# Optimization experiments

Measured on AMD Instinct MI355X. Metric: run time of the kernel, lower is better.

The kernel has to match this reference:

```python
import jax, jax.numpy as jnp
from jax import lax
import numpy as np

D = 1024   # hidden_size
N = 8      # num_experts
K = 2      # num_chosen_experts
KS = 1     # num_shared_experts
H = 2 * D  # hidden_ratio * D
B, S = 2, 1024


def setup_inputs() -> dict:
    key = jax.random.key(0)
    k1, k2, k3, k4 = jax.random.split(key, 4)
    scale = 1.0 / np.sqrt(D).astype(np.float32)
    x = jax.random.normal(k1, (B, S, D), dtype=jnp.float32)
    Wg = jax.random.normal(k2, (D, N), dtype=jnp.float32) * scale
    Wl1 = jax.random.normal(k3, (N, D, 2 * H), dtype=jnp.float32) * scale
    Wl2 = jax.random.normal(k4, (N, H, D), dtype=jnp.float32) * scale
    return {"x_BSD": x, "Wg_DN": Wg, "Wl1_ND2H": Wl1, "Wl2_NHD": Wl2}


def _moe(x_BSD, Wg_DN, Wl1_ND2H, Wl2_NHD):
    b, s, d = x_BSD.shape
    x_MD = x_BSD.reshape(b * s, d)            # [M, D]
    Nr = N - KS                               # number of routed experts

    # --- gating (softmax path) ---
    s_raw_MN = x_MD @ Wg_DN                   # [M, N]
    routed = jax.nn.softmax(s_raw_MN[:, :Nr].astype(jnp.float32), axis=-1)
    shared = jax.nn.softmax(s_raw_MN[:, Nr:].astype(jnp.float32), axis=-1)

    # biases for routed experts are zero at init -> topk on raw softmax scores
    _, idx_MK = lax.top_k(routed, K - KS)     # [M, K-KS]
    mask = jnp.sum(jax.nn.one_hot(idx_MK, Nr, dtype=jnp.float32), axis=1)  # [M, Nr]
    sel = routed * mask
    routed_n = sel / jnp.sum(sel, axis=-1, keepdims=True)   # renormalize selected gates
    shared_n = shared / jnp.sum(shared, axis=-1, keepdims=True)
    gates_MN = jnp.concatenate([routed_n, shared_n], axis=-1).astype(x_MD.dtype)  # [M, N]

    # --- experts: gather-free dense combine; gates are exactly 0 for unselected experts ---
    def step(y_MD, inp):
        w1_D2H, w2_HD, g_M = inp
        z = x_MD @ w1_D2H                     # [M, 2H]
        a, bgate = jnp.split(z, 2, axis=-1)
        h = jax.nn.silu(bgate) * a            # SwiGLU
        return y_MD + g_M[:, None] * (h @ w2_HD), None

    y0 = jnp.zeros_like(x_MD)
    y_MD, _ = lax.scan(step, y0, (Wl1_ND2H, Wl2_NHD, gates_MN.T))
    return y_MD.reshape(b, s, d)


def reference(x_BSD, Wg_DN, Wl1_ND2H, Wl2_NHD):
    return _moe(x_BSD, Wg_DN, Wl1_ND2H, Wl2_NHD)
```

## Files before the change

kernel.cpp:

```cpp
#include <hip/hip_runtime.h>
#include <stdint.h>


typedef __bf16 bf16x8 __attribute__((ext_vector_type(8)));
typedef float f32x4 __attribute__((ext_vector_type(4)));

typedef __attribute__((address_space(1))) const void gvoid_t;
typedef __attribute__((address_space(3))) void lvoid_t;

__device__ __forceinline__ void gload16(void* lds, const void* g) {
  __builtin_amdgcn_global_load_lds((gvoid_t*)g, (lvoid_t*)lds, 16, 0, 0);
}

__device__ __forceinline__ uint16_t f2bf(float f) {
  union { float f; uint32_t u; } v; v.f = f;
  uint32_t u = v.u + 0x7fffu + ((v.u >> 16) & 1u);
  return (uint16_t)(u >> 16);
}

#define S_VMCNT12() asm volatile("s_waitcnt vmcnt(12)" ::: "memory")
#define S_VMCNT16() asm volatile("s_waitcnt vmcnt(16)" ::: "memory")
#define S_VMCNT0()  asm volatile("s_waitcnt vmcnt(0)" ::: "memory")
#define S_LGKM0()   asm volatile("s_waitcnt lgkmcnt(0)" ::: "memory")
#define S_BAR()     __builtin_amdgcn_s_barrier()

#define CVT_PK(dst, lo, hi) \
  asm("v_cvt_pk_bf16_f32 %0, %1, %2" : "=v"(dst) : "v"(lo), "v"(hi))

__global__ __launch_bounds__(256) void gate_kernel(const float* __restrict__ x,
                                                   const float* __restrict__ Wg,
                                                   uint16_t* __restrict__ xbf,
                                                   int* __restrict__ idx) {
  int wid = threadIdx.x >> 6, lane = threadIdx.x & 63;
  int m = blockIdx.x * 4 + wid;
  const float* xr = x + (size_t)m * 1024;
  uint16_t* xbr = xbf + (size_t)m * 1024;
  float acc[8] = {0.f, 0.f, 0.f, 0.f, 0.f, 0.f, 0.f, 0.f};
  for (int it = 0; it < 4; ++it) {
    int dbase = it * 256 + lane * 4;
    float4 xv = *reinterpret_cast<const float4*>(xr + dbase);
    ushort4 o;
    o.x = f2bf(xv.x); o.y = f2bf(xv.y); o.z = f2bf(xv.z); o.w = f2bf(xv.w);
    *reinterpret_cast<ushort4*>(xbr + dbase) = o;
    const float* xp = reinterpret_cast<const float*>(&xv);
    for (int dd = 0; dd < 4; ++dd) {
      float xs = xp[dd];
      float4 w0 = *reinterpret_cast<const float4*>(Wg + (size_t)(dbase + dd) * 8);
      float4 w1 = *reinterpret_cast<const float4*>(Wg + (size_t)(dbase + dd) * 8 + 4);
      acc[0] += xs * w0.x; acc[1] += xs * w0.y; acc[2] += xs * w0.z; acc[3] += xs * w0.w;
      acc[4] += xs * w1.x; acc[5] += xs * w1.y; acc[6] += xs * w1.z; acc[7] += xs * w1.w;
    }
  }
  for (int j = 0; j < 7; ++j)
    for (int off = 32; off; off >>= 1)
      acc[j] += __shfl_xor(acc[j], off);
  if (lane == 0) {
    int best = 0; float bv = acc[0];
    for (int j = 1; j < 7; ++j) if (acc[j] > bv) { bv = acc[j]; best = j; }
    idx[m] = best;
  }
}

__global__ __launch_bounds__(256) void compact_kernel(const int* __restrict__ idx,
                                                      int* __restrict__ soff,
                                                      int* __restrict__ scnt,
                                                      int* __restrict__ rowmap,
                                                      int* __restrict__ tokrow) {
  __shared__ int hist[256][7];
  __shared__ int cnts[7];
  __shared__ int off[7];
  int t = threadIdx.x;
  int e8[8];
  int lh[7] = {0, 0, 0, 0, 0, 0, 0};
#pragma unroll
  for (int i = 0; i < 8; ++i) { int e = idx[t * 8 + i]; e8[i] = e; lh[e]++; }
#pragma unroll
  for (int e = 0; e < 7; ++e) hist[t][e] = lh[e];
  __syncthreads();
  if (t < 7) {
    int run = 0;
    for (int i = 0; i < 256; ++i) { int v = hist[i][t]; hist[i][t] = run; run += v; }
    cnts[t] = run;
  }
  __syncthreads();
  if (t == 0) {
    int run = 0;
    for (int e = 0; e < 7; ++e) { off[e] = run; soff[e] = run; scnt[e] = cnts[e]; run += cnts[e]; }
    soff[7] = 0; scnt[7] = 2048;
  }
  __syncthreads();
  int pos[7];
#pragma unroll
  for (int e = 0; e < 7; ++e) pos[e] = off[e] + hist[t][e];
#pragma unroll
  for (int i = 0; i < 8; ++i) {
    int m = t * 8 + i, e = e8[i];
    int r = pos[e]++;
    rowmap[r] = m;
    tokrow[m] = r;
  }
}

__global__ __launch_bounds__(256, 2) void ffn1_kernel(
    const uint16_t* __restrict__ xbf,
    const float* __restrict__ W1,
    const int* __restrict__ soff, const int* __restrict__ scnt,
    const int* __restrict__ rowmap,
    uint16_t* __restrict__ h)
{
  int by = blockIdx.y;
  int seg, rt;
  if (by < 42) { seg = by / 6; rt = by % 6; } else { seg = 7; rt = by - 42; }
  int cnt = scnt[seg];
  if (rt * 128 >= cnt) return;
  int base = (seg == 7) ? 2048 : soff[seg];
  int rbase = (seg == 7) ? 0 : soff[seg];
  int n0 = blockIdx.x * 64;

  __shared__ uint16_t lds[2][16384];

  int t = threadIdx.x, lane = t & 63, w = t >> 6;
  int trow = w * 8 + ((t >> 3) & 7);
  int slot = (t & 7) ^ (trow & 7);

  const uint16_t* aptr[4];
#pragma unroll
  for (int i = 0; i < 4; ++i) {
    int rl = i * 32 + trow;
    int rr = rt * 128 + rl; if (rr >= cnt) rr = cnt - 1;
    int tok = (seg == 7) ? rr : rowmap[rbase + rr];
    aptr[i] = xbf + (size_t)tok * 1024 + slot * 8;
  }
  auto stageA = [&](int buf, int kt) {
    uint16_t* L = lds[buf];
#pragma unroll
    for (int i = 0; i < 4; ++i) gload16(&L[(i * 32 + trow) * 64 + (t & 7) * 8], aptr[i] + kt * 64);
  };

  const float* w1f = W1 + (size_t)seg * (1024u * 4096u);
  int kg = t >> 5;
  int n4 = (t & 31) * 4;
  int gcol = (n4 < 64) ? (n0 + n4) : (2048 + n0 + n4 - 64);
  const float* bsrc = w1f + (size_t)(kg * 8) * 4096 + gcol;
  int bwoff[4];
#pragma unroll
  for (int j = 0; j < 4; ++j) {
    int cl = n4 + j;
    int sw = cl ^ ((cl >> 2) & 7);
    bwoff[j] = 8192 + kg * 1024 + sw * 8;
  }
  f32x4 P0[8], P1[8];
  auto issueB = [&](f32x4 (&P)[8], int kt) {
    const float* p = bsrc + (size_t)kt * 64 * 4096;
#pragma unroll
    for (int i = 0; i < 8; ++i) P[i] = *reinterpret_cast<const f32x4*>(p + (size_t)i * 4096);
  };
  auto writeB = [&](f32x4 (&P)[8], int buf) {
    uint16_t* L = lds[buf];
#pragma unroll
    for (int j = 0; j < 4; ++j) {
      uint32_t q0, q1, q2, q3;
      CVT_PK(q0, P[0][j], P[1][j]);
      CVT_PK(q1, P[2][j], P[3][j]);
      CVT_PK(q2, P[4][j], P[5][j]);
      CVT_PK(q3, P[6][j], P[7][j]);
      uint4 v; v.x = q0; v.y = q1; v.z = q2; v.w = q3;
      *reinterpret_cast<uint4*>(&L[bwoff[j]]) = v;
    }
  };

  int wr = (w >> 1) & 1, wc = w & 1;
  int l15 = lane & 15, lk = lane >> 4;
  int boffA[2], boffB[2];
#pragma unroll
  for (int n = 0; n < 2; ++n) {
    int cl = wc * 32 + n * 16 + l15;
    boffA[n] = 8192 + (cl ^ ((cl >> 2) & 7)) * 8;
    cl += 64;
    boffB[n] = 8192 + (cl ^ ((cl >> 2) & 7)) * 8;
  }

  f32x4 acca[4][2] = {};
  f32x4 accb[4][2] = {};

  auto compute = [&](int buf) {
    const uint16_t* L = lds[buf];
#pragma unroll
    for (int g = 0; g < 2; ++g) {
      __builtin_amdgcn_s_setprio(1);
      bf16x8 af[4];
#pragma unroll
      for (int m = 0; m < 4; ++m) {
        int row = wr * 64 + m * 16 + l15;
        int p = (g * 4 + lk) ^ (row & 7);
        af[m] = *reinterpret_cast<const bf16x8*>(&L[row * 64 + p * 8]);
      }
#pragma unroll
      for (int n = 0; n < 2; ++n) {
        int ks = (g * 4 + lk) * 1024;
        bf16x8 ba = *reinterpret_cast<const bf16x8*>(&L[boffA[n] + ks]);
        bf16x8 bb = *reinterpret_cast<const bf16x8*>(&L[boffB[n] + ks]);
#pragma unroll
        for (int m = 0; m < 4; ++m) {
          acca[m][n] = __builtin_amdgcn_mfma_f32_16x16x32_bf16(af[m], ba, acca[m][n], 0, 0, 0);
          accb[m][n] = __builtin_amdgcn_mfma_f32_16x16x32_bf16(af[m], bb, accb[m][n], 0, 0, 0);
        }
      }
      __builtin_amdgcn_s_setprio(0);
    }
  };

  const int NT = 16;
  issueB(P0, 0); stageA(0, 0);
  issueB(P1, 1); stageA(1, 1);
  S_VMCNT16();
  writeB(P0, 0);
  issueB(P0, 2);
  S_LGKM0();

#pragma unroll 1
  for (int kt = 0; kt < NT; kt += 2) {
    if (kt < NT - 2) S_VMCNT12(); else S_VMCNT0();
    S_BAR();
    compute(0);
    if (kt < NT - 1) writeB(P1, 1);
    S_LGKM0(); S_BAR();
    if (kt < NT - 3) issueB(P1, kt + 3);
    if (kt < NT - 2) stageA(0, kt + 2);
    int ko = kt + 1;
    if (ko < NT - 2) S_VMCNT12(); else S_VMCNT0();
    S_BAR();
    compute(1);
    if (ko < NT - 1) writeB(P0, 0);
    S_LGKM0(); S_BAR();
    if (ko < NT - 3) issueB(P0, ko + 3);
    if (ko < NT - 2) stageA(1, ko + 2);
  }

#pragma unroll
  for (int m = 0; m < 4; ++m)
#pragma unroll
    for (int n = 0; n < 2; ++n) {
      int col = n0 + wc * 32 + n * 16 + l15;
#pragma unroll
      for (int j = 0; j < 4; ++j) {
        int row = rt * 128 + wr * 64 + m * 16 + lk * 4 + j;
        if (row < cnt) {
          float a = acca[m][n][j], b = accb[m][n][j];
          float sv = b / (1.0f + __expf(-b));
          h[(size_t)(base + row) * 2048 + col] = f2bf(sv * a);
        }
      }
    }
}

__global__ __launch_bounds__(256, 2) void ffn2_kernel(
    const uint16_t* __restrict__ h,
    const float* __restrict__ W2,
    const int* __restrict__ soff, const int* __restrict__ scnt,
    float* __restrict__ y,
    float* __restrict__ yr)
{
  int by = blockIdx.y;
  int seg, rt;
  if (by < 42) { seg = by / 6; rt = by % 6; } else { seg = 7; rt = by - 42; }
  int cnt = scnt[seg];
  if (rt * 128 >= cnt) return;
  int base = (seg == 7) ? 2048 : soff[seg];
  int obase = (seg == 7) ? 0 : soff[seg];
  int n0 = blockIdx.x * 128;

  __shared__ uint16_t lds[2][16384];

  int t = threadIdx.x, lane = t & 63, w = t >> 6;
  int trow = w * 8 + ((t >> 3) & 7);
  int slot = (t & 7) ^ (trow & 7);

  const uint16_t* aptr[4];
#pragma unroll
  for (int i = 0; i < 4; ++i) {
    int rl = i * 32 + trow;
    int rr = rt * 128 + rl; if (rr >= cnt) rr = cnt - 1;
    aptr[i] = h + (size_t)(base + rr) * 2048 + slot * 8;
  }
  auto stageA = [&](int buf, int kt) {
    uint16_t* L = lds[buf];
#pragma unroll
    for (int i = 0; i < 4; ++i) gload16(&L[(i * 32 + trow) * 64 + (t & 7) * 8], aptr[i] + kt * 64);
  };

  const float* w2f = W2 + (size_t)seg * (2048u * 1024u);
  int kg = t >> 5;
  int n4 = (t & 31) * 4;
  const float* bsrc = w2f + (size_t)(kg * 8) * 1024 + n0 + n4;
  int bwoff[4];
#pragma unroll
  for (int j = 0; j < 4; ++j) {
    int cl = n4 + j;
    int sw = cl ^ ((cl >> 2) & 7);
    bwoff[j] = 8192 + kg * 1024 + sw * 8;
  }
  f32x4 P0[8], P1[8];
  auto issueB = [&](f32x4 (&P)[8], int kt) {
    const float* p = bsrc + (size_t)kt * 64 * 1024;
#pragma unroll
    for (int i = 0; i < 8; ++i) P[i] = *reinterpret_cast<const f32x4*>(p + (size_t)i * 1024);
  };
  auto writeB = [&](f32x4 (&P)[8], int buf) {
    uint16_t* L = lds[buf];
#pragma unroll
    for (int j = 0; j < 4; ++j) {
      uint32_t q0, q1, q2, q3;
      CVT_PK(q0, P[0][j], P[1][j]);
      CVT_PK(q1, P[2][j], P[3][j]);
      CVT_PK(q2, P[4][j], P[5][j]);
      CVT_PK(q3, P[6][j], P[7][j]);
      uint4 v; v.x = q0; v.y = q1; v.z = q2; v.w = q3;
      *reinterpret_cast<uint4*>(&L[bwoff[j]]) = v;
    }
  };

  int wr = (w >> 1) & 1, wc = w & 1;
  int l15 = lane & 15, lk = lane >> 4;
  int boff[4];
#pragma unroll
  for (int n = 0; n < 4; ++n) {
    int cl = wc * 64 + n * 16 + l15;
    boff[n] = 8192 + (cl ^ ((cl >> 2) & 7)) * 8;
  }

  f32x4 acc[4][4] = {};

  auto compute = [&](int buf) {
    const uint16_t* L = lds[buf];
#pragma unroll
    for (int g = 0; g < 2; ++g) {
      __builtin_amdgcn_s_setprio(1);
      bf16x8 af[4];
#pragma unroll
      for (int m = 0; m < 4; ++m) {
        int row = wr * 64 + m * 16 + l15;
        int p = (g * 4 + lk) ^ (row & 7);
        af[m] = *reinterpret_cast<const bf16x8*>(&L[row * 64 + p * 8]);
      }
#pragma unroll
      for (int n = 0; n < 4; ++n) {
        bf16x8 bfr = *reinterpret_cast<const bf16x8*>(&L[boff[n] + (g * 4 + lk) * 1024]);
#pragma unroll
        for (int m = 0; m < 4; ++m)
          acc[m][n] = __builtin_amdgcn_mfma_f32_16x16x32_bf16(af[m], bfr, acc[m][n], 0, 0, 0);
      }
      __builtin_amdgcn_s_setprio(0);
    }
  };

  const int NT = 32;
  issueB(P0, 0); stageA(0, 0);
  issueB(P1, 1); stageA(1, 1);
  S_VMCNT16();
  writeB(P0, 0);
  issueB(P0, 2);
  S_LGKM0();

#pragma unroll 1
  for (int kt = 0; kt < NT; kt += 2) {
    if (kt < NT - 2) S_VMCNT12(); else S_VMCNT0();
    S_BAR();
    compute(0);
    if (kt < NT - 1) writeB(P1, 1);
    S_LGKM0(); S_BAR();
    if (kt < NT - 3) issueB(P1, kt + 3);
    if (kt < NT - 2) stageA(0, kt + 2);
    int ko = kt + 1;
    if (ko < NT - 2) S_VMCNT12(); else S_VMCNT0();
    S_BAR();
    compute(1);
    if (ko < NT - 1) writeB(P0, 0);
    S_LGKM0(); S_BAR();
    if (ko < NT - 3) issueB(P0, ko + 3);
    if (ko < NT - 2) stageA(1, ko + 2);
  }

#pragma unroll
  for (int m = 0; m < 4; ++m)
#pragma unroll
    for (int n = 0; n < 4; ++n) {
      int col = n0 + wc * 64 + n * 16 + l15;
#pragma unroll
      for (int j = 0; j < 4; ++j) {
        int row = rt * 128 + wr * 64 + m * 16 + lk * 4 + j;
        if (row < cnt) {
          if (seg == 7) y[(size_t)row * 1024 + col] = acc[m][n][j];
          else          yr[(size_t)(obase + row) * 1024 + col] = acc[m][n][j];
        }
      }
    }
}

__global__ __launch_bounds__(256) void combine_kernel(const float* __restrict__ yr,
                                                      const int* __restrict__ tokrow,
                                                      float* __restrict__ y) {
  int m = blockIdx.x;
  int d = threadIdx.x * 4;
  int r = tokrow[m];
  float4 a = *reinterpret_cast<const float4*>(yr + (size_t)r * 1024 + d);
  float4 o = *reinterpret_cast<const float4*>(y + (size_t)m * 1024 + d);
  o.x += a.x; o.y += a.y; o.z += a.z; o.w += a.w;
  *reinterpret_cast<float4*>(y + (size_t)m * 1024 + d) = o;
}

extern "C" void kernel_launch(void* const* d_in, const int* in_sizes, int n_in,
                              void* d_out, int out_size, void* d_ws, size_t ws_size,
                              hipStream_t stream)
{
  const float* x   = (const float*)d_in[0];
  const float* Wg  = (const float*)d_in[1];
  const float* Wl1 = (const float*)d_in[2];
  const float* Wl2 = (const float*)d_in[3];
  float* y = (float*)d_out;
  char* ws = (char*)d_ws;

  uint16_t* xbf = (uint16_t*)(ws);
  uint16_t* h   = (uint16_t*)(ws + (4ull  << 20));
  float*    yr  = (float*)   (ws + (20ull << 20));
  int* idx    = (int*)(ws + (28ull << 20));
  int* tokrow = idx + 2048;
  int* soff   = tokrow + 2048;
  int* scnt   = soff + 8;
  int* rowmap = scnt + 8;

  gate_kernel<<<512, 256, 0, stream>>>(x, Wg, xbf, idx);
  compact_kernel<<<1, 256, 0, stream>>>(idx, soff, scnt, rowmap, tokrow);
  ffn1_kernel<<<dim3(32, 58), 256, 0, stream>>>(xbf, Wl1, soff, scnt, rowmap, h);
  ffn2_kernel<<<dim3(8, 58), 256, 0, stream>>>(h, Wl2, soff, scnt, y, yr);
  combine_kernel<<<2048, 256, 0, stream>>>(yr, tokrow, y);
}
```

Before: 129.4 us.

## Fuse routed-expert combine into FFN2 epilogue via rowmap scatter-add

```diff
diff --git a/kernel.cpp b/kernel.cpp
--- a/kernel.cpp
+++ b/kernel.cpp
@@ -64,8 +64,7 @@
 __global__ __launch_bounds__(256) void compact_kernel(const int* __restrict__ idx,
                                                       int* __restrict__ soff,
                                                       int* __restrict__ scnt,
-                                                      int* __restrict__ rowmap,
-                                                      int* __restrict__ tokrow) {
+                                                      int* __restrict__ rowmap) {
   __shared__ int hist[256][7];
   __shared__ int cnts[7];
   __shared__ int off[7];
@@ -95,9 +94,7 @@
 #pragma unroll
   for (int i = 0; i < 8; ++i) {
     int m = t * 8 + i, e = e8[i];
-    int r = pos[e]++;
-    rowmap[r] = m;
-    tokrow[m] = r;
+    rowmap[pos[e]++] = m;
   }
 }
 
@@ -176,8 +173,8 @@
   for (int n = 0; n < 2; ++n) {
     int cl = wc * 32 + n * 16 + l15;
     boffA[n] = 8192 + (cl ^ ((cl >> 2) & 7)) * 8;
-    cl += 64;
-    boffB[n] = 8192 + (cl ^ ((cl >> 2) & 7)) * 8;
+    int cb = cl + 64;
+    boffB[n] = 8192 + (cb ^ ((cb >> 2) & 7)) * 8;
   }
 
   f32x4 acca[4][2] = {};
@@ -254,20 +251,21 @@
     }
 }
 
+template <int SHARED>
 __global__ __launch_bounds__(256, 2) void ffn2_kernel(
     const uint16_t* __restrict__ h,
     const float* __restrict__ W2,
     const int* __restrict__ soff, const int* __restrict__ scnt,
-    float* __restrict__ y,
-    float* __restrict__ yr)
+    const int* __restrict__ rowmap,
+    float* __restrict__ y)
 {
   int by = blockIdx.y;
   int seg, rt;
-  if (by < 42) { seg = by / 6; rt = by % 6; } else { seg = 7; rt = by - 42; }
+  if (SHARED) { seg = 7; rt = by; } else { seg = by / 6; rt = by % 6; }
   int cnt = scnt[seg];
   if (rt * 128 >= cnt) return;
   int base = (seg == 7) ? 2048 : soff[seg];
-  int obase = (seg == 7) ? 0 : soff[seg];
+  int rbase = soff[seg];
   int n0 = blockIdx.x * 128;
 
   __shared__ uint16_t lds[2][16384];
@@ -390,23 +388,15 @@
       for (int j = 0; j < 4; ++j) {
         int row = rt * 128 + wr * 64 + m * 16 + lk * 4 + j;
         if (row < cnt) {
-          if (seg == 7) y[(size_t)row * 1024 + col] = acc[m][n][j];
-          else          yr[(size_t)(obase + row) * 1024 + col] = acc[m][n][j];
+          if (SHARED) {
+            y[(size_t)row * 1024 + col] = acc[m][n][j];
+          } else {
+            int tok = rowmap[rbase + row];
+            y[(size_t)tok * 1024 + col] += acc[m][n][j];
+          }
         }
       }
     }
-}
-
-__global__ __launch_bounds__(256) void combine_kernel(const float* __restrict__ yr,
-                                                      const int* __restrict__ tokrow,
-                                                      float* __restrict__ y) {
-  int m = blockIdx.x;
-  int d = threadIdx.x * 4;
-  int r = tokrow[m];
-  float4 a = *reinterpret_cast<const float4*>(yr + (size_t)r * 1024 + d);
-  float4 o = *reinterpret_cast<const float4*>(y + (size_t)m * 1024 + d);
-  o.x += a.x; o.y += a.y; o.z += a.z; o.w += a.w;
-  *reinterpret_cast<float4*>(y + (size_t)m * 1024 + d) = o;
 }
 
 extern "C" void kernel_launch(void* const* d_in, const int* in_sizes, int n_in,
@@ -422,16 +412,14 @@
 
   uint16_t* xbf = (uint16_t*)(ws);
   uint16_t* h   = (uint16_t*)(ws + (4ull  << 20));
-  float*    yr  = (float*)   (ws + (20ull << 20));
-  int* idx    = (int*)(ws + (28ull << 20));
-  int* tokrow = idx + 2048;
-  int* soff   = tokrow + 2048;
+  int* idx    = (int*)(ws + (20ull << 20));
+  int* soff   = idx + 2048;
   int* scnt   = soff + 8;
   int* rowmap = scnt + 8;
 
   gate_kernel<<<512, 256, 0, stream>>>(x, Wg, xbf, idx);
-  compact_kernel<<<1, 256, 0, stream>>>(idx, soff, scnt, rowmap, tokrow);
+  compact_kernel<<<1, 256, 0, stream>>>(idx, soff, scnt, rowmap);
   ffn1_kernel<<<dim3(32, 58), 256, 0, stream>>>(xbf, Wl1, soff, scnt, rowmap, h);
-  ffn2_kernel<<<dim3(8, 58), 256, 0, stream>>>(h, Wl2, soff, scnt, y, yr);
-  combine_kernel<<<2048, 256, 0, stream>>>(yr, tokrow, y);
-}
+  ffn2_kernel<1><<<dim3(8, 16), 256, 0, stream>>>(h, Wl2, soff, scnt, rowmap, y);
+  ffn2_kernel<0><<<dim3(8, 42), 256, 0, stream>>>(h, Wl2, soff, scnt, rowmap, y);
+}
```

Result: slower. 181.5 us (+40.3%).
